# Kernel optimization log

Measured on AMD Instinct MI355X. Metric: run time of the kernel, lower is better.

The kernel has to match this reference:

```python
import jax, jax.numpy as jnp
import numpy as np

D_MODEL, N_HEADS, D_K, D_V = 512, 8, 32, 32
LN_EPS = 1e-5


def setup_inputs() -> dict:
    key = jax.random.key(0)
    ks = jax.random.split(key, 12)
    B, L = 4, 2048
    inner = N_HEADS * D_K
    s_in = 1.0 / np.sqrt(D_MODEL)
    s_fc = 1.0 / np.sqrt(inner)
    return {
        "q": jax.random.normal(ks[0], (B, L, D_MODEL), jnp.float32),
        "k": jax.random.normal(ks[1], (B, L, D_MODEL), jnp.float32),
        "v": jax.random.normal(ks[2], (B, L, D_MODEL), jnp.float32),
        "Wq": jax.random.normal(ks[3], (inner, D_MODEL), jnp.float32) * s_in,
        "bq": jax.random.normal(ks[4], (inner,), jnp.float32) * 0.01,
        "Wk": jax.random.normal(ks[5], (inner, D_MODEL), jnp.float32) * s_in,
        "bk": jax.random.normal(ks[6], (inner,), jnp.float32) * 0.01,
        "Wv": jax.random.normal(ks[7], (N_HEADS * D_V, D_MODEL), jnp.float32) * s_in,
        "bv": jax.random.normal(ks[8], (N_HEADS * D_V,), jnp.float32) * 0.01,
        "Wfc": jax.random.normal(ks[9], (D_MODEL, N_HEADS * D_V), jnp.float32) * s_fc,
        "bfc": jax.random.normal(ks[10], (D_MODEL,), jnp.float32) * 0.01,
        "gamma": jnp.ones((D_MODEL,), jnp.float32),
        "beta": jnp.zeros((D_MODEL,), jnp.float32),
    }


def reference(q, k, v, Wq, bq, Wk, bk, Wv, bv, Wfc, bfc, gamma, beta):
    n, l, _ = q.shape
    # Projection output interpreted as (..., d_k, n_heads): head idx is fastest dim
    def split_heads(x, W, b, dh):
        p = x @ W.T + b                     # [n, l, dh*H]
        return p.reshape(n, x.shape[1], dh, N_HEADS).transpose(0, 3, 1, 2)  # [n,H,l,dh]

    qh = split_heads(q, Wq, bq, D_K)
    kh = split_heads(k, Wk, bk, D_K)
    vh = split_heads(v, Wv, bv, D_V)

    scale = 1.0 / jnp.sqrt(jnp.asarray(D_K, q.dtype))
    scores = jnp.einsum('nhqd,nhkd->nhqk', qh, kh) * scale  # [n,H,L,L]
    att = jax.nn.softmax(scores, axis=-1)
    out = jnp.einsum('nhqk,nhkd->nhqd', att, vh)             # [n,H,L,d_v]
    out = out.transpose(0, 2, 1, 3).reshape(n, l, N_HEADS * D_V)

    fc = out @ Wfc.T + bfc
    x = fc + q  # residual
    mean = jnp.mean(x, axis=-1, keepdims=True)
    var = jnp.mean(jnp.square(x - mean), axis=-1, keepdims=True)
    return gamma * (x - mean) / jnp.sqrt(var + LN_EPS) + beta
```

## Files before the change

### kernel.cpp

```cpp
#include <hip/hip_runtime.h>
#include <math.h>

constexpr int Bn = 4, Ln = 2048, DM = 512, NH = 8, DKv = 32, INNER = 256;
constexpr int TTOK = Bn * Ln;
constexpr size_t HEAD_ELEMS = (size_t)Bn * NH * Ln * DKv;


typedef short short8 __attribute__((ext_vector_type(8)));
typedef short short4v __attribute__((ext_vector_type(4)));
typedef float floatx4 __attribute__((ext_vector_type(4)));
typedef float floatx16 __attribute__((ext_vector_type(16)));

constexpr size_t WB_OFF  = 12536832;
constexpr size_t WFCB_OFF = WB_OFF + 3 * 131072;

constexpr float C1 = 0.25505654f;

__device__ inline short f2bf(float x) {
  unsigned u = __builtin_bit_cast(unsigned, x);
  unsigned r = (u + 0x7FFFu + ((u >> 16) & 1u)) >> 16;
  return (short)r;
}

__global__ __launch_bounds__(256) void cvtw_kernel(
    const float* __restrict__ Wq, const float* __restrict__ Wk,
    const float* __restrict__ Wv, const float* __restrict__ Wfc,
    short* __restrict__ Wb, short* __restrict__ Wfcb)
{
  const int z = blockIdx.y;
  const float* src = z == 0 ? Wq : (z == 1 ? Wk : (z == 2 ? Wv : Wfc));
  short* dst = z < 3 ? Wb + (size_t)z * 131072 : Wfcb;
  const int idx = (blockIdx.x * 256 + threadIdx.x) * 4;
  float4 x = *(const float4*)&src[idx];
  *(short4v*)&dst[idx] = (short4v){f2bf(x.x), f2bf(x.y), f2bf(x.z), f2bf(x.w)};
}

__global__ __launch_bounds__(256) void proj_kernel(
    const float* __restrict__ q, const float* __restrict__ k, const float* __restrict__ v,
    const short* __restrict__ Wb,
    const float* __restrict__ bq, const float* __restrict__ bk,
    const float* __restrict__ bv,
    short* __restrict__ ws)
{
  const int mat = blockIdx.y;
  const float* X    = mat == 0 ? q  : (mat == 1 ? k  : v);
  const short* W    = Wb + (size_t)mat * 131072;
  const float* bias = mat == 0 ? bq : (mat == 1 ? bk : bv);
  short* outp = ws + (size_t)mat * HEAD_ELEMS;

  const int t0 = blockIdx.x * 64;
  const int tid = threadIdx.x;
  const int col = tid & 15;
  const int quad = (tid & 63) >> 4;
  const int w = tid >> 6;

  __shared__ short smem[23040];
  short* Xs  = smem;
  short* Wsh = smem + 64 * 72;

  floatx16 accv;
  floatx4 acc[16];
#pragma unroll
  for (int nj = 0; nj < 16; ++nj) acc[nj] = (floatx4){0.f, 0.f, 0.f, 0.f};
  (void)accv;

  float4 xr[4];
  short8 wr[8];
  auto loadX = [&](int k0) {
#pragma unroll
    for (int j = 0; j < 4; ++j) {
      const int i = tid + j * 256, row = i >> 4, c4 = i & 15;
      xr[j] = *(const float4*)&X[(size_t)(t0 + row) * DM + k0 + c4 * 4];
    }
  };
  auto loadW = [&](int k0) {
#pragma unroll
    for (int j = 0; j < 8; ++j) {
      const int s = tid + j * 256, jrow = s >> 3, c8 = s & 7;
      const int wrow = ((jrow & 31) << 3) + (jrow >> 5);
      wr[j] = *(const short8*)&W[(size_t)wrow * DM + k0 + c8 * 8];
    }
  };

  loadX(0);
  loadW(0);

  for (int kc = 0; kc < 8; ++kc) {
#pragma unroll
    for (int j = 0; j < 4; ++j) {
      const int i = tid + j * 256, row = i >> 4, c4 = i & 15;
      *(short4v*)&Xs[row * 72 + c4 * 4] =
          (short4v){f2bf(xr[j].x), f2bf(xr[j].y), f2bf(xr[j].z), f2bf(xr[j].w)};
    }
#pragma unroll
    for (int j = 0; j < 8; ++j) {
      const int s = tid + j * 256, jrow = s >> 3, c8 = s & 7;
      *(short8*)&Wsh[jrow * 72 + c8 * 8] = wr[j];
    }
    __syncthreads();
    if (kc < 7) {
      loadX((kc + 1) * 64);
      loadW((kc + 1) * 64);
    }
#pragma unroll
    for (int ks = 0; ks < 2; ++ks) {
      short8 a = *(const short8*)&Xs[(w * 16 + col) * 72 + ks * 32 + quad * 8];
#pragma unroll
      for (int nj = 0; nj < 16; ++nj) {
        short8 b = *(const short8*)&Wsh[(nj * 16 + col) * 72 + ks * 32 + quad * 8];
        acc[nj] = __builtin_amdgcn_mfma_f32_16x16x32_bf16(a, b, acc[nj], 0, 0, 0);
      }
    }
    __syncthreads();
  }

  short* Ct = smem;
  const int n = t0 >> 11, llb = t0 & (Ln - 1);

  if (mat < 2) {
#pragma unroll
    for (int nj = 0; nj < 16; ++nj) {
      const int j = nj * 16 + col;
      const int c = ((j & 31) << 3) + (j >> 5);
      const float bi = bias[c];
#pragma unroll
      for (int r = 0; r < 4; ++r) {
        float pv = acc[nj][r] + bi;
        if (mat == 0) pv *= C1;
        Ct[(w * 16 + quad * 4 + r) * 268 + j] = f2bf(pv);
      }
    }
    __syncthreads();
#pragma unroll
    for (int it = 0; it < 8; ++it) {
      const int cid = tid + it * 256;
      const int h = cid >> 8, tok = (cid >> 2) & 63, o = cid & 3;
      short8 val = *(const short8*)&Ct[tok * 268 + h * 32 + o * 8];
      *(short8*)&outp[((size_t)(n * NH + h) * Ln + llb + tok) * DKv + o * 8] = val;
    }
  } else {
#pragma unroll
    for (int nj = 0; nj < 16; ++nj) {
      const int j = nj * 16 + col;
      const int c = ((j & 31) << 3) + (j >> 5);
      const float bi = bias[c];
      short4v pk = (short4v){f2bf(acc[nj][0] + bi), f2bf(acc[nj][1] + bi),
                             f2bf(acc[nj][2] + bi), f2bf(acc[nj][3] + bi)};
      *(short4v*)&Ct[j * 72 + w * 16 + quad * 4] = pk;
    }
    __syncthreads();
#pragma unroll
    for (int it = 0; it < 8; ++it) {
      const int cid = tid + it * 256;
      const int j = cid >> 3, to = cid & 7;
      const int h = j >> 5, d = j & 31;
      short8 val = *(const short8*)&Ct[j * 72 + to * 8];
      *(short8*)&outp[((size_t)(n * NH + h) * DKv + d) * Ln + llb + to * 8] = val;
    }
  }
}

__global__ __launch_bounds__(256) void attn_kernel(const short* __restrict__ ws,
                                                   short* __restrict__ O2b)
{
  const int vid = blockIdx.x + 16 * blockIdx.y;
  const int xcd = vid & 7, jj = vid >> 3;
  const int bh = xcd * 4 + (jj >> 4);
  const int qblk = jj & 15;

  const int n = bh >> 3, h = bh & 7;
  const int tid = threadIdx.x;
  const int lane = tid & 63;
  const int col = lane & 31;
  const int hf = lane >> 5;
  const int w = tid >> 6;
  const int qi = qblk * 128 + w * 32 + col;

  const short* Qh = ws;
  const short* Kg = ws + HEAD_ELEMS + (size_t)bh * Ln * DKv;
  const short* Vg = ws + 2 * HEAD_ELEMS + (size_t)bh * DKv * Ln;

  __shared__ short Ks[2][128 * 40];
  __shared__ short Vs[2][32 * 136];

  short8 aq[2];
#pragma unroll
  for (int c = 0; c < 2; ++c)
    aq[c] = *(const short8*)&Qh[(size_t)bh * Ln * DKv + (size_t)qi * DKv + c * 16 + hf * 8];

  short8 ones;
#pragma unroll
  for (int j = 0; j < 8; ++j) ones[j] = (short)0x3F80;

  floatx16 o, ol;
#pragma unroll
  for (int i = 0; i < 16; ++i) { o[i] = 0.f; ol[i] = 0.f; }

  const int kg = tid >> 1, khalf = tid & 1;
  const int krow = (kg & ~12) | ((kg & 4) << 1) | ((kg & 8) >> 1);
  const int kst = krow * 40 + khalf * 16;
  const int vd = tid >> 3, vkb = tid & 7;
  const int vst = vd * 136 + vkb * 16;

  short8 kr0 = *(const short8*)(Kg + kg * 32 + khalf * 16);
  short8 kr1 = *(const short8*)(Kg + kg * 32 + khalf * 16 + 8);
  short8 vr0 = *(const short8*)(Vg + (size_t)vd * Ln + vkb * 16);
  short8 vr1 = *(const short8*)(Vg + (size_t)vd * Ln + vkb * 16 + 8);

  for (int kt = 0; kt < 16; ++kt) {
    short* ksb = Ks[kt & 1];
    short* vsb = Vs[kt & 1];
    *(short8*)&ksb[kst] = kr0;
    *(short8*)&ksb[kst + 8] = kr1;
    *(short8*)&vsb[vst] = vr0;
    *(short8*)&vsb[vst + 8] = vr1;
    __syncthreads();
    if (kt < 15) {
      kr0 = *(const short8*)(Kg + (size_t)(kt + 1) * 4096 + kg * 32 + khalf * 16);
      kr1 = *(const short8*)(Kg + (size_t)(kt + 1) * 4096 + kg * 32 + khalf * 16 + 8);
      vr0 = *(const short8*)(Vg + (size_t)vd * Ln + (kt + 1) * 128 + vkb * 16);
      vr1 = *(const short8*)(Vg + (size_t)vd * Ln + (kt + 1) * 128 + vkb * 16 + 8);
    }

#pragma unroll
    for (int cc = 0; cc < 4; ++cc) {
      floatx16 st;
#pragma unroll
      for (int i = 0; i < 16; ++i) st[i] = 0.f;
      short8 kf0 = *(const short8*)&ksb[(cc * 32 + col) * 40 + hf * 8];
      short8 kf1 = *(const short8*)&ksb[(cc * 32 + col) * 40 + 16 + hf * 8];
      st = __builtin_amdgcn_mfma_f32_32x32x16_bf16(kf0, aq[0], st, 0, 0, 0);
      st = __builtin_amdgcn_mfma_f32_32x32x16_bf16(kf1, aq[1], st, 0, 0, 0);

      float p[16];
#pragma unroll
      for (int i = 0; i < 16; ++i) p[i] = __builtin_amdgcn_exp2f(st[i]);
      short8 pf[2];
#pragma unroll
      for (int half = 0; half < 2; ++half) {
        unsigned u[4];
#pragma unroll
        for (int j = 0; j < 4; ++j)
          u[j] = __builtin_amdgcn_perm(
              __builtin_bit_cast(unsigned, p[half * 8 + 2 * j + 1]),
              __builtin_bit_cast(unsigned, p[half * 8 + 2 * j]), 0x07060302u);
        uint4 uu = make_uint4(u[0], u[1], u[2], u[3]);
        pf[half] = __builtin_bit_cast(short8, uu);
      }

      ol = __builtin_amdgcn_mfma_f32_32x32x16_bf16(ones, pf[0], ol, 0, 0, 0);
      ol = __builtin_amdgcn_mfma_f32_32x32x16_bf16(ones, pf[1], ol, 0, 0, 0);

      short8 va0 = *(const short8*)&vsb[col * 136 + cc * 32 + hf * 8];
      short8 va1 = *(const short8*)&vsb[col * 136 + cc * 32 + 16 + hf * 8];
      o = __builtin_amdgcn_mfma_f32_32x32x16_bf16(va0, pf[0], o, 0, 0, 0);
      o = __builtin_amdgcn_mfma_f32_32x32x16_bf16(va1, pf[1], o, 0, 0, 0);
    }
  }

  const float inv = 1.f / ol[0];
  short* dst = &O2b[((size_t)n * Ln + qi) * INNER + h * DKv];
#pragma unroll
  for (int g4 = 0; g4 < 4; ++g4) {
    short4v pk = (short4v){f2bf(o[g4 * 4 + 0] * inv), f2bf(o[g4 * 4 + 1] * inv),
                           f2bf(o[g4 * 4 + 2] * inv), f2bf(o[g4 * 4 + 3] * inv)};
    *(short4v*)&dst[8 * g4 + 4 * hf] = pk;
  }
}

__global__ __launch_bounds__(256) void fcln_kernel(
    const short* __restrict__ O2b, const short* __restrict__ Wfcb,
    const float* __restrict__ bfc, const float* __restrict__ qin,
    const float* __restrict__ gamma, const float* __restrict__ beta,
    float* __restrict__ outp)
{
  const int t0 = blockIdx.x * 16;
  const int tid = threadIdx.x;
  const int col = tid & 15;
  const int quad = (tid & 63) >> 4;
  const int w = tid >> 6;

  __shared__ short As[16 * 264];
  __shared__ float sred[2][16][4];

  {
    const int row = tid >> 4, k16 = tid & 15;
    *(short8*)&As[row * 264 + k16 * 16] =
        *(const short8*)&O2b[(size_t)(t0 + row) * INNER + k16 * 16];
    *(short8*)&As[row * 264 + k16 * 16 + 8] =
        *(const short8*)&O2b[(size_t)(t0 + row) * INNER + k16 * 16 + 8];
  }
  __syncthreads();

  const short* Wp = Wfcb + (size_t)(w * 128 + col) * INNER + quad * 8;

  floatx4 acc[8];
#pragma unroll
  for (int nj = 0; nj < 8; ++nj) acc[nj] = (floatx4){0.f, 0.f, 0.f, 0.f};

#pragma unroll
  for (int ks = 0; ks < 8; ++ks) {
    short8 a = *(const short8*)&As[col * 264 + ks * 32 + quad * 8];
#pragma unroll
    for (int nj = 0; nj < 8; ++nj) {
      short8 b = *(const short8*)&Wp[(size_t)nj * 16 * INNER + ks * 32];
      acc[nj] = __builtin_amdgcn_mfma_f32_16x16x32_bf16(a, b, acc[nj], 0, 0, 0);
    }
  }

  float s1[4], s2[4];
#pragma unroll
  for (int r = 0; r < 4; ++r) { s1[r] = 0.f; s2[r] = 0.f; }

#pragma unroll
  for (int nj = 0; nj < 8; ++nj) {
    const int c = w * 128 + nj * 16 + col;
    const float bi = bfc[c];
#pragma unroll
    for (int r = 0; r < 4; ++r) {
      const int t = t0 + quad * 4 + r;
      float x = acc[nj][r] + bi + qin[(size_t)t * DM + c];
      acc[nj][r] = x;
      s1[r] += x;
      s2[r] += x * x;
    }
  }
#pragma unroll
  for (int r = 0; r < 4; ++r) {
#pragma unroll
    for (int off = 1; off <= 8; off <<= 1) {
      s1[r] += __shfl_xor(s1[r], off);
      s2[r] += __shfl_xor(s2[r], off);
    }
  }
  if (col == 0) {
#pragma unroll
    for (int r = 0; r < 4; ++r) {
      sred[0][quad * 4 + r][w] = s1[r];
      sred[1][quad * 4 + r][w] = s2[r];
    }
  }
  __syncthreads();

  float mean[4], rstd[4];
#pragma unroll
  for (int r = 0; r < 4; ++r) {
    const int tk = quad * 4 + r;
    const float S1 = sred[0][tk][0] + sred[0][tk][1] + sred[0][tk][2] + sred[0][tk][3];
    const float S2 = sred[1][tk][0] + sred[1][tk][1] + sred[1][tk][2] + sred[1][tk][3];
    mean[r] = S1 * (1.f / 512.f);
    const float var = S2 * (1.f / 512.f) - mean[r] * mean[r];
    rstd[r] = rsqrtf(var + 1e-5f);
  }

#pragma unroll
  for (int nj = 0; nj < 8; ++nj) {
    const int c = w * 128 + nj * 16 + col;
    const float g = gamma[c], bb = beta[c];
#pragma unroll
    for (int r = 0; r < 4; ++r) {
      const int t = t0 + quad * 4 + r;
      outp[(size_t)t * DM + c] = g * (acc[nj][r] - mean[r]) * rstd[r] + bb;
    }
  }
}

extern "C" void kernel_launch(void* const* d_in, const int* in_sizes, int n_in,
                              void* d_out, int out_size, void* d_ws, size_t ws_size,
                              hipStream_t stream) {
  const float* q     = (const float*)d_in[0];
  const float* k     = (const float*)d_in[1];
  const float* v     = (const float*)d_in[2];
  const float* Wq    = (const float*)d_in[3];
  const float* bq    = (const float*)d_in[4];
  const float* Wk    = (const float*)d_in[5];
  const float* bk    = (const float*)d_in[6];
  const float* Wv    = (const float*)d_in[7];
  const float* bv    = (const float*)d_in[8];
  const float* Wfc   = (const float*)d_in[9];
  const float* bfc   = (const float*)d_in[10];
  const float* gamma = (const float*)d_in[11];
  const float* beta  = (const float*)d_in[12];

  short* wsS  = (short*)d_ws;
  short* O2b  = wsS + 3 * HEAD_ELEMS;
  short* Wb   = wsS + WB_OFF;
  short* Wfcb = wsS + WFCB_OFF;

  cvtw_kernel<<<dim3(128, 4), 256, 0, stream>>>(Wq, Wk, Wv, Wfc, Wb, Wfcb);

  dim3 gp(TTOK / 64, 3);
  proj_kernel<<<gp, 256, 0, stream>>>(q, k, v, Wb, bq, bk, bv, wsS);

  dim3 gatt(Ln / 128, Bn * NH);
  attn_kernel<<<gatt, 256, 0, stream>>>(wsS, O2b);

  fcln_kernel<<<dim3(TTOK / 16), 256, 0, stream>>>(O2b, Wfcb, bfc, q, gamma, beta,
                                                   (float*)d_out);
}
```

Measured before the change: 174.5 us.

## Split projection, attention and FC/LN work across more blocks and waves

The projection kernel now splits the output heads into two halves via a new grid dimension, doubling the block count with half the accumulators and shared memory per block. Attention uses 64-query blocks, and the waves of each block split the key range into two halves, merged at the end through a shared-memory reduction. The row-sum is now computed with scalar adds instead of a ones-MFMA. The FC/LayerNorm kernel moves to 512 threads with fewer columns per wave. The aim is more parallelism and occupancy, at the cost of re-reading X per head-half, extra reduction and sync overhead, and larger LayerNorm partial sums.

```diff
diff --git a/kernel.cpp b/kernel.cpp
--- a/kernel.cpp
+++ b/kernel.cpp
@@ -42,7 +42,8 @@
     const float* __restrict__ bv,
     short* __restrict__ ws)
 {
-  const int mat = blockIdx.y;
+  const int mat = blockIdx.z;
+  const int hp  = blockIdx.y;
   const float* X    = mat == 0 ? q  : (mat == 1 ? k  : v);
   const short* W    = Wb + (size_t)mat * 131072;
   const float* bias = mat == 0 ? bq : (mat == 1 ? bk : bv);
@@ -54,18 +55,16 @@
   const int quad = (tid & 63) >> 4;
   const int w = tid >> 6;
 
-  __shared__ short smem[23040];
+  __shared__ short smem[13824];
   short* Xs  = smem;
   short* Wsh = smem + 64 * 72;
 
-  floatx16 accv;
-  floatx4 acc[16];
-#pragma unroll
-  for (int nj = 0; nj < 16; ++nj) acc[nj] = (floatx4){0.f, 0.f, 0.f, 0.f};
-  (void)accv;
+  floatx4 acc[8];
+#pragma unroll
+  for (int nj = 0; nj < 8; ++nj) acc[nj] = (floatx4){0.f, 0.f, 0.f, 0.f};
 
   float4 xr[4];
-  short8 wr[8];
+  short8 wr[4];
   auto loadX = [&](int k0) {
 #pragma unroll
     for (int j = 0; j < 4; ++j) {
@@ -75,9 +74,9 @@
   };
   auto loadW = [&](int k0) {
 #pragma unroll
-    for (int j = 0; j < 8; ++j) {
+    for (int j = 0; j < 4; ++j) {
       const int s = tid + j * 256, jrow = s >> 3, c8 = s & 7;
-      const int wrow = ((jrow & 31) << 3) + (jrow >> 5);
+      const int wrow = ((jrow & 31) << 3) + 4 * hp + (jrow >> 5);
       wr[j] = *(const short8*)&W[(size_t)wrow * DM + k0 + c8 * 8];
     }
   };
@@ -93,7 +92,7 @@
           (short4v){f2bf(xr[j].x), f2bf(xr[j].y), f2bf(xr[j].z), f2bf(xr[j].w)};
     }
 #pragma unroll
-    for (int j = 0; j < 8; ++j) {
+    for (int j = 0; j < 4; ++j) {
       const int s = tid + j * 256, jrow = s >> 3, c8 = s & 7;
       *(short8*)&Wsh[jrow * 72 + c8 * 8] = wr[j];
     }
@@ -106,7 +105,7 @@
     for (int ks = 0; ks < 2; ++ks) {
       short8 a = *(const short8*)&Xs[(w * 16 + col) * 72 + ks * 32 + quad * 8];
 #pragma unroll
-      for (int nj = 0; nj < 16; ++nj) {
+      for (int nj = 0; nj < 8; ++nj) {
         short8 b = *(const short8*)&Wsh[(nj * 16 + col) * 72 + ks * 32 + quad * 8];
         acc[nj] = __builtin_amdgcn_mfma_f32_16x16x32_bf16(a, b, acc[nj], 0, 0, 0);
       }
@@ -119,30 +118,31 @@
 
   if (mat < 2) {
 #pragma unroll
-    for (int nj = 0; nj < 16; ++nj) {
+    for (int nj = 0; nj < 8; ++nj) {
       const int j = nj * 16 + col;
-      const int c = ((j & 31) << 3) + (j >> 5);
+      const int c = ((j & 31) << 3) + 4 * hp + (j >> 5);
       const float bi = bias[c];
 #pragma unroll
       for (int r = 0; r < 4; ++r) {
         float pv = acc[nj][r] + bi;
         if (mat == 0) pv *= C1;
-        Ct[(w * 16 + quad * 4 + r) * 268 + j] = f2bf(pv);
+        Ct[(w * 16 + quad * 4 + r) * 136 + j] = f2bf(pv);
       }
     }
     __syncthreads();
 #pragma unroll
-    for (int it = 0; it < 8; ++it) {
+    for (int it = 0; it < 4; ++it) {
       const int cid = tid + it * 256;
-      const int h = cid >> 8, tok = (cid >> 2) & 63, o = cid & 3;
-      short8 val = *(const short8*)&Ct[tok * 268 + h * 32 + o * 8];
+      const int h_loc = cid >> 8, tok = (cid >> 2) & 63, o = cid & 3;
+      short8 val = *(const short8*)&Ct[tok * 136 + h_loc * 32 + o * 8];
+      const int h = 4 * hp + h_loc;
       *(short8*)&outp[((size_t)(n * NH + h) * Ln + llb + tok) * DKv + o * 8] = val;
     }
   } else {
 #pragma unroll
-    for (int nj = 0; nj < 16; ++nj) {
+    for (int nj = 0; nj < 8; ++nj) {
       const int j = nj * 16 + col;
-      const int c = ((j & 31) << 3) + (j >> 5);
+      const int c = ((j & 31) << 3) + 4 * hp + (j >> 5);
       const float bi = bias[c];
       short4v pk = (short4v){f2bf(acc[nj][0] + bi), f2bf(acc[nj][1] + bi),
                              f2bf(acc[nj][2] + bi), f2bf(acc[nj][3] + bi)};
@@ -150,10 +150,10 @@
     }
     __syncthreads();
 #pragma unroll
-    for (int it = 0; it < 8; ++it) {
+    for (int it = 0; it < 4; ++it) {
       const int cid = tid + it * 256;
       const int j = cid >> 3, to = cid & 7;
-      const int h = j >> 5, d = j & 31;
+      const int h = 4 * hp + (j >> 5), d = j & 31;
       short8 val = *(const short8*)&Ct[j * 72 + to * 8];
       *(short8*)&outp[((size_t)(n * NH + h) * DKv + d) * Ln + llb + to * 8] = val;
     }
@@ -163,10 +163,10 @@
 __global__ __launch_bounds__(256) void attn_kernel(const short* __restrict__ ws,
                                                    short* __restrict__ O2b)
 {
-  const int vid = blockIdx.x + 16 * blockIdx.y;
+  const int vid = blockIdx.x + 32 * blockIdx.y;
   const int xcd = vid & 7, jj = vid >> 3;
-  const int bh = xcd * 4 + (jj >> 4);
-  const int qblk = jj & 15;
+  const int bh = xcd * 4 + (jj >> 5);
+  const int qblk = jj & 31;
 
   const int n = bh >> 3, h = bh & 7;
   const int tid = threadIdx.x;
@@ -174,53 +174,54 @@
   const int col = lane & 31;
   const int hf = lane >> 5;
   const int w = tid >> 6;
-  const int qi = qblk * 128 + w * 32 + col;
+  const int g = w >> 1;
+  const int qs = w & 1;
+  const int qi = qblk * 64 + qs * 32 + col;
+  const int kb0 = g * 1024;
 
   const short* Qh = ws;
   const short* Kg = ws + HEAD_ELEMS + (size_t)bh * Ln * DKv;
   const short* Vg = ws + 2 * HEAD_ELEMS + (size_t)bh * DKv * Ln;
 
-  __shared__ short Ks[2][128 * 40];
-  __shared__ short Vs[2][32 * 136];
+  __shared__ short smem[18944];
+  short* ksb = smem + g * 9472;
+  short* vsb = ksb + 5120;
 
   short8 aq[2];
 #pragma unroll
   for (int c = 0; c < 2; ++c)
     aq[c] = *(const short8*)&Qh[(size_t)bh * Ln * DKv + (size_t)qi * DKv + c * 16 + hf * 8];
 
-  short8 ones;
-#pragma unroll
-  for (int j = 0; j < 8; ++j) ones[j] = (short)0x3F80;
-
-  floatx16 o, ol;
-#pragma unroll
-  for (int i = 0; i < 16; ++i) { o[i] = 0.f; ol[i] = 0.f; }
-
-  const int kg = tid >> 1, khalf = tid & 1;
+  floatx16 o;
+#pragma unroll
+  for (int i = 0; i < 16; ++i) o[i] = 0.f;
+  float lacc = 0.f;
+
+  const int gtid = tid & 127;
+  const int kg = gtid;
   const int krow = (kg & ~12) | ((kg & 4) << 1) | ((kg & 8) >> 1);
-  const int kst = krow * 40 + khalf * 16;
-  const int vd = tid >> 3, vkb = tid & 7;
-  const int vst = vd * 136 + vkb * 16;
-
-  short8 kr0 = *(const short8*)(Kg + kg * 32 + khalf * 16);
-  short8 kr1 = *(const short8*)(Kg + kg * 32 + khalf * 16 + 8);
-  short8 vr0 = *(const short8*)(Vg + (size_t)vd * Ln + vkb * 16);
-  short8 vr1 = *(const short8*)(Vg + (size_t)vd * Ln + vkb * 16 + 8);
-
-  for (int kt = 0; kt < 16; ++kt) {
-    short* ksb = Ks[kt & 1];
-    short* vsb = Vs[kt & 1];
-    *(short8*)&ksb[kst] = kr0;
-    *(short8*)&ksb[kst + 8] = kr1;
-    *(short8*)&vsb[vst] = vr0;
-    *(short8*)&vsb[vst + 8] = vr1;
-    __syncthreads();
-    if (kt < 15) {
-      kr0 = *(const short8*)(Kg + (size_t)(kt + 1) * 4096 + kg * 32 + khalf * 16);
-      kr1 = *(const short8*)(Kg + (size_t)(kt + 1) * 4096 + kg * 32 + khalf * 16 + 8);
-      vr0 = *(const short8*)(Vg + (size_t)vd * Ln + (kt + 1) * 128 + vkb * 16);
-      vr1 = *(const short8*)(Vg + (size_t)vd * Ln + (kt + 1) * 128 + vkb * 16 + 8);
-    }
+  const int vd = gtid >> 2, vq = gtid & 3;
+
+  short8 kr[4], vr[4];
+  auto prefetch = [&](int kt) {
+    const size_t kbase = (size_t)(kb0 + kt * 128);
+#pragma unroll
+    for (int s = 0; s < 4; ++s)
+      kr[s] = *(const short8*)(Kg + (kbase + kg) * 32 + s * 8);
+#pragma unroll
+    for (int s = 0; s < 4; ++s)
+      vr[s] = *(const short8*)(Vg + (size_t)vd * Ln + kbase + vq * 32 + s * 8);
+  };
+
+  prefetch(0);
+
+  for (int kt = 0; kt < 8; ++kt) {
+#pragma unroll
+    for (int s = 0; s < 4; ++s) *(short8*)&ksb[krow * 40 + s * 8] = kr[s];
+#pragma unroll
+    for (int s = 0; s < 4; ++s) *(short8*)&vsb[vd * 136 + vq * 32 + s * 8] = vr[s];
+    __syncthreads();
+    if (kt < 7) prefetch(kt + 1);
 
 #pragma unroll
     for (int cc = 0; cc < 4; ++cc) {
@@ -235,40 +236,64 @@
       float p[16];
 #pragma unroll
       for (int i = 0; i < 16; ++i) p[i] = __builtin_amdgcn_exp2f(st[i]);
+
+      float ls = 0.f;
+#pragma unroll
+      for (int i = 0; i < 16; ++i) ls += p[i];
+      lacc += ls;
+
       short8 pf[2];
 #pragma unroll
       for (int half = 0; half < 2; ++half) {
-        unsigned u[4];
-#pragma unroll
-        for (int j = 0; j < 4; ++j)
-          u[j] = __builtin_amdgcn_perm(
-              __builtin_bit_cast(unsigned, p[half * 8 + 2 * j + 1]),
-              __builtin_bit_cast(unsigned, p[half * 8 + 2 * j]), 0x07060302u);
-        uint4 uu = make_uint4(u[0], u[1], u[2], u[3]);
+        unsigned u0 = __builtin_amdgcn_perm(
+            __builtin_bit_cast(unsigned, p[half * 8 + 1]),
+            __builtin_bit_cast(unsigned, p[half * 8 + 0]), 0x07060302u);
+        unsigned u1 = __builtin_amdgcn_perm(
+            __builtin_bit_cast(unsigned, p[half * 8 + 3]),
+            __builtin_bit_cast(unsigned, p[half * 8 + 2]), 0x07060302u);
+        unsigned u2 = __builtin_amdgcn_perm(
+            __builtin_bit_cast(unsigned, p[half * 8 + 5]),
+            __builtin_bit_cast(unsigned, p[half * 8 + 4]), 0x07060302u);
+        unsigned u3 = __builtin_amdgcn_perm(
+            __builtin_bit_cast(unsigned, p[half * 8 + 7]),
+            __builtin_bit_cast(unsigned, p[half * 8 + 6]), 0x07060302u);
+        uint4 uu = make_uint4(u0, u1, u2, u3);
         pf[half] = __builtin_bit_cast(short8, uu);
       }
-
-      ol = __builtin_amdgcn_mfma_f32_32x32x16_bf16(ones, pf[0], ol, 0, 0, 0);
-      ol = __builtin_amdgcn_mfma_f32_32x32x16_bf16(ones, pf[1], ol, 0, 0, 0);
 
       short8 va0 = *(const short8*)&vsb[col * 136 + cc * 32 + hf * 8];
       short8 va1 = *(const short8*)&vsb[col * 136 + cc * 32 + 16 + hf * 8];
       o = __builtin_amdgcn_mfma_f32_32x32x16_bf16(va0, pf[0], o, 0, 0, 0);
       o = __builtin_amdgcn_mfma_f32_32x32x16_bf16(va1, pf[1], o, 0, 0, 0);
     }
-  }
-
-  const float inv = 1.f / ol[0];
-  short* dst = &O2b[((size_t)n * Ln + qi) * INNER + h * DKv];
-#pragma unroll
-  for (int g4 = 0; g4 < 4; ++g4) {
-    short4v pk = (short4v){f2bf(o[g4 * 4 + 0] * inv), f2bf(o[g4 * 4 + 1] * inv),
-                           f2bf(o[g4 * 4 + 2] * inv), f2bf(o[g4 * 4 + 3] * inv)};
-    *(short4v*)&dst[8 * g4 + 4 * hf] = pk;
-  }
-}
-
-__global__ __launch_bounds__(256) void fcln_kernel(
+    __syncthreads();
+  }
+
+  float* red = (float*)smem;
+  if (tid >= 128) {
+    const int idx = tid - 128;
+#pragma unroll
+    for (int i = 0; i < 16; ++i) red[idx * 17 + i] = o[i];
+    red[idx * 17 + 16] = lacc;
+  }
+  __syncthreads();
+  if (tid < 128) {
+#pragma unroll
+    for (int i = 0; i < 16; ++i) o[i] += red[tid * 17 + i];
+    lacc += red[tid * 17 + 16];
+    const float ltot = lacc + __shfl_xor(lacc, 32);
+    const float inv = 1.f / ltot;
+    short* dst = &O2b[((size_t)n * Ln + qi) * INNER + h * DKv];
+#pragma unroll
+    for (int g4 = 0; g4 < 4; ++g4) {
+      short4v pk = (short4v){f2bf(o[g4 * 4 + 0] * inv), f2bf(o[g4 * 4 + 1] * inv),
+                             f2bf(o[g4 * 4 + 2] * inv), f2bf(o[g4 * 4 + 3] * inv)};
+      *(short4v*)&dst[8 * g4 + 4 * hf] = pk;
+    }
+  }
+}
+
+__global__ __launch_bounds__(512) void fcln_kernel(
     const short* __restrict__ O2b, const short* __restrict__ Wfcb,
     const float* __restrict__ bfc, const float* __restrict__ qin,
     const float* __restrict__ gamma, const float* __restrict__ beta,
@@ -281,28 +306,26 @@
   const int w = tid >> 6;
 
   __shared__ short As[16 * 264];
-  __shared__ float sred[2][16][4];
+  __shared__ float sred[2][16][8];
 
   {
-    const int row = tid >> 4, k16 = tid & 15;
-    *(short8*)&As[row * 264 + k16 * 16] =
-        *(const short8*)&O2b[(size_t)(t0 + row) * INNER + k16 * 16];
-    *(short8*)&As[row * 264 + k16 * 16 + 8] =
-        *(const short8*)&O2b[(size_t)(t0 + row) * INNER + k16 * 16 + 8];
+    const int row = tid >> 5, k8 = tid & 31;
+    *(short8*)&As[row * 264 + k8 * 8] =
+        *(const short8*)&O2b[(size_t)(t0 + row) * INNER + k8 * 8];
   }
   __syncthreads();
 
-  const short* Wp = Wfcb + (size_t)(w * 128 + col) * INNER + quad * 8;
-
-  floatx4 acc[8];
-#pragma unroll
-  for (int nj = 0; nj < 8; ++nj) acc[nj] = (floatx4){0.f, 0.f, 0.f, 0.f};
+  const short* Wp = Wfcb + (size_t)(w * 64 + col) * INNER + quad * 8;
+
+  floatx4 acc[4];
+#pragma unroll
+  for (int nj = 0; nj < 4; ++nj) acc[nj] = (floatx4){0.f, 0.f, 0.f, 0.f};
 
 #pragma unroll
   for (int ks = 0; ks < 8; ++ks) {
     short8 a = *(const short8*)&As[col * 264 + ks * 32 + quad * 8];
 #pragma unroll
-    for (int nj = 0; nj < 8; ++nj) {
+    for (int nj = 0; nj < 4; ++nj) {
       short8 b = *(const short8*)&Wp[(size_t)nj * 16 * INNER + ks * 32];
       acc[nj] = __builtin_amdgcn_mfma_f32_16x16x32_bf16(a, b, acc[nj], 0, 0, 0);
     }
@@ -313,8 +336,8 @@
   for (int r = 0; r < 4; ++r) { s1[r] = 0.f; s2[r] = 0.f; }
 
 #pragma unroll
-  for (int nj = 0; nj < 8; ++nj) {
-    const int c = w * 128 + nj * 16 + col;
+  for (int nj = 0; nj < 4; ++nj) {
+    const int c = w * 64 + nj * 16 + col;
     const float bi = bfc[c];
 #pragma unroll
     for (int r = 0; r < 4; ++r) {
@@ -346,16 +369,17 @@
 #pragma unroll
   for (int r = 0; r < 4; ++r) {
     const int tk = quad * 4 + r;
-    const float S1 = sred[0][tk][0] + sred[0][tk][1] + sred[0][tk][2] + sred[0][tk][3];
-    const float S2 = sred[1][tk][0] + sred[1][tk][1] + sred[1][tk][2] + sred[1][tk][3];
+    float S1 = 0.f, S2 = 0.f;
+#pragma unroll
+    for (int ww = 0; ww < 8; ++ww) { S1 += sred[0][tk][ww]; S2 += sred[1][tk][ww]; }
     mean[r] = S1 * (1.f / 512.f);
     const float var = S2 * (1.f / 512.f) - mean[r] * mean[r];
     rstd[r] = rsqrtf(var + 1e-5f);
   }
 
 #pragma unroll
-  for (int nj = 0; nj < 8; ++nj) {
-    const int c = w * 128 + nj * 16 + col;
+  for (int nj = 0; nj < 4; ++nj) {
+    const int c = w * 64 + nj * 16 + col;
     const float g = gamma[c], bb = beta[c];
 #pragma unroll
     for (int r = 0; r < 4; ++r) {
@@ -389,12 +413,12 @@
 
   cvtw_kernel<<<dim3(128, 4), 256, 0, stream>>>(Wq, Wk, Wv, Wfc, Wb, Wfcb);
 
-  dim3 gp(TTOK / 64, 3);
+  dim3 gp(TTOK / 64, 2, 3);
   proj_kernel<<<gp, 256, 0, stream>>>(q, k, v, Wb, bq, bk, bv, wsS);
 
-  dim3 gatt(Ln / 128, Bn * NH);
+  dim3 gatt(32, 32);
   attn_kernel<<<gatt, 256, 0, stream>>>(wsS, O2b);
 
-  fcln_kernel<<<dim3(TTOK / 16), 256, 0, stream>>>(O2b, Wfcb, bfc, q, gamma, beta,
+  fcln_kernel<<<dim3(TTOK / 16), 512, 0, stream>>>(O2b, Wfcb, bfc, q, gamma, beta,
                                                    (float*)d_out);
 }
```

Measured after the change: 176.9 us. No clear change (+1.3%).
